# Performance work log

Hardware: AMD Instinct MI355X
Metric: run time of the kernel (lower is better)

Reference implementation:

```python
import jax, jax.numpy as jnp
import numpy as np

HEADS = 12  # hard-coded in the original module (rearrange h=12, temp shape (12,1))


def setup_inputs() -> dict:
    key = jax.random.key(0)
    k1, k2, k3 = jax.random.split(key, 3)
    B, C, H, W = 16, 768, 64, 64  # C = 3*dim with dim=256; per-head d = C/12 = 64
    x = jax.random.normal(k1, (B, C, H, W), dtype=jnp.float32)
    W_qkv = jax.random.normal(k2, (C, C), dtype=jnp.float32) * 0.02
    W_out = jax.random.normal(k3, (C, C), dtype=jnp.float32) * 0.02
    temp = jnp.ones((HEADS, 1), dtype=jnp.float32)
    return {"x": x, "W_qkv": W_qkv, "W_out": W_out, "temp": temp}


def reference(x, W_qkv, W_out, temp):
    B, C, H, W = x.shape
    N = H * W
    d = C // HEADS
    # to_3d: b c h w -> b (h w) c
    x3 = jnp.transpose(x, (0, 2, 3, 1)).reshape(B, N, C)
    # qkv projection (nn.Linear, no bias): x @ W^T
    w = (x3 @ W_qkv.T).reshape(B, N, HEADS, d).transpose(0, 2, 1, 3)  # [B, H, N, d]
    # F.normalize along the token axis (dim=-2), eps=1e-12
    norm = jnp.sqrt(jnp.sum(w * w, axis=2, keepdims=True))
    w_normed = w / jnp.maximum(norm, 1e-12)
    w_sq = w_normed ** 2
    # per-(head, token) stats, scaled by learned temp, softmax over HEADS axis (dim=1!)
    logits = jnp.sum(w_sq, axis=-1) * temp          # [B, H, N] (temp [12,1] broadcasts)
    Pi = jax.nn.softmax(logits, axis=1)             # softmax over heads
    Pi_n = Pi / (jnp.sum(Pi, axis=-1, keepdims=True) + 1e-8)
    # dots: [B,H,1,N] @ [B,H,N,d] -> [B,H,1,d]
    dots = jnp.einsum('bhn,bhnd->bhd', Pi_n, w ** 2)[:, :, None, :]
    attn = 1.0 / (1.0 + dots)                       # [B, H, 1, d]
    out = -(w * Pi[..., None]) * attn               # [B, H, N, d]
    # b h n d -> b n (h d)
    out = out.transpose(0, 2, 1, 3).reshape(B, N, C)
    out = out @ W_out.T
    # b (h w) c -> b c h w
    return out.reshape(B, H, W, C).transpose(0, 3, 1, 2)
```

## Files before the change

kernel.cpp:

```cpp
#include <hip/hip_runtime.h>
#include <stdint.h>

#define B_ 16
#define C_ 768
#define N_ 4096
#define HEADS_ 12

typedef __attribute__((ext_vector_type(4))) float f32x4;
typedef __attribute__((ext_vector_type(8))) short s16x8;

__device__ __forceinline__ ushort f2bf(float f){
  union { float f; uint32_t u; } v; v.f = f;
  uint32_t u = v.u;
  uint32_t r = (u + 0x7fffu + ((u >> 16) & 1u)) >> 16;
  return (ushort)r;
}
__device__ __forceinline__ float bf2f(ushort h){
  union { uint32_t u; float f; } v; v.u = ((uint32_t)h) << 16;
  return v.f;
}

__global__ __launch_bounds__(256) void k_convert(const float* __restrict__ src,
                                                 ushort* __restrict__ dst, int n){
  int i = (blockIdx.x * 256 + threadIdx.x) * 4;
  if (i < n){
    float4 v = *(const float4*)(src + i);
    ushort4 u;
    u.x = f2bf(v.x); u.y = f2bf(v.y); u.z = f2bf(v.z); u.w = f2bf(v.w);
    *(ushort4*)(dst + i) = u;
  }
}

__global__ __launch_bounds__(256) void k_transpose(const float* __restrict__ x,
                                                   ushort* __restrict__ xT){
  __shared__ ushort tile[64][72];
  int b = blockIdx.z;
  int n0 = blockIdx.x * 64;
  int k0 = blockIdx.y * 64;
  int t = threadIdx.x;
  const float* xb = x + (size_t)b * C_ * N_;
  #pragma unroll
  for (int p = 0; p < 4; ++p){
    int krow = (t >> 4) + p * 16;
    int nn = (t & 15) * 4;
    float4 v = *(const float4*)(xb + (size_t)(k0 + krow) * N_ + n0 + nn);
    tile[nn + 0][krow] = f2bf(v.x);
    tile[nn + 1][krow] = f2bf(v.y);
    tile[nn + 2][krow] = f2bf(v.z);
    tile[nn + 3][krow] = f2bf(v.w);
  }
  __syncthreads();
  ushort* dst = xT + (size_t)b * N_ * C_;
  #pragma unroll
  for (int p = 0; p < 4; ++p){
    int nrow = (t >> 4) + p * 16;
    int kk = (t & 15) * 4;
    ushort4 u = *(ushort4*)&tile[nrow][kk];
    *(ushort4*)(dst + (size_t)(n0 + nrow) * C_ + k0 + kk) = u;
  }
}

#define BM 128
#define BN 128
#define BK 64
#define LDK 72

__global__ __launch_bounds__(256, 2) void k_gemm1(const ushort* __restrict__ xT,
                                                  const ushort* __restrict__ wq,
                                                  ushort* __restrict__ w,
                                                  float* __restrict__ colnorm2){
  __shared__ ushort As[BM * LDK];
  __shared__ ushort Bs[BN * LDK];
  int b = blockIdx.z;
  int n0 = blockIdx.x * BM;
  int c0 = blockIdx.y * BN;
  int t = threadIdx.x;
  int lane = t & 63, wv = t >> 6;
  int wm = wv >> 1, wn = wv & 1;
  int col = lane & 15, quad = lane >> 4;
  const ushort* Ag = xT + (size_t)b * N_ * C_ + (size_t)n0 * C_;
  const ushort* Bg = wq + (size_t)c0 * C_;
  f32x4 acc[4][4] = {};
  for (int kt = 0; kt < C_; kt += BK){
    #pragma unroll
    for (int p = 0; p < 4; ++p){
      int q = t + 256 * p;
      int row = q >> 3, ch = q & 7;
      uint4 va = *(const uint4*)(Ag + (size_t)row * C_ + kt + ch * 8);
      *(uint4*)&As[row * LDK + ch * 8] = va;
      uint4 vb = *(const uint4*)(Bg + (size_t)row * C_ + kt + ch * 8);
      *(uint4*)&Bs[row * LDK + ch * 8] = vb;
    }
    __syncthreads();
    #pragma unroll
    for (int ks = 0; ks < 2; ++ks){
      s16x8 af[4], bf[4];
      #pragma unroll
      for (int mt = 0; mt < 4; ++mt)
        af[mt] = *(s16x8*)&As[(wm * 64 + mt * 16 + col) * LDK + ks * 32 + quad * 8];
      #pragma unroll
      for (int nt = 0; nt < 4; ++nt)
        bf[nt] = *(s16x8*)&Bs[(wn * 64 + nt * 16 + col) * LDK + ks * 32 + quad * 8];
      #pragma unroll
      for (int mt = 0; mt < 4; ++mt)
        #pragma unroll
        for (int nt = 0; nt < 4; ++nt)
          acc[mt][nt] = __builtin_amdgcn_mfma_f32_16x16x32_bf16(af[mt], bf[nt], acc[mt][nt], 0, 0, 0);
    }
    __syncthreads();
  }
  ushort* wb = w + (size_t)b * N_ * C_;
  #pragma unroll
  for (int nt = 0; nt < 4; ++nt){
    int cc = c0 + wn * 64 + nt * 16 + col;
    float ss = 0.f;
    #pragma unroll
    for (int mt = 0; mt < 4; ++mt){
      #pragma unroll
      for (int r = 0; r < 4; ++r){
        int nn = n0 + wm * 64 + mt * 16 + quad * 4 + r;
        float v = acc[mt][nt][r];
        wb[(size_t)nn * C_ + cc] = f2bf(v);
        ss += v * v;
      }
    }
    ss += __shfl_xor(ss, 16);
    ss += __shfl_xor(ss, 32);
    if (quad == 0) atomicAdd(colnorm2 + b * C_ + cc, ss);
  }
}

__global__ __launch_bounds__(256) void k_stats(const ushort* __restrict__ w,
                                               const float* __restrict__ colnorm2,
                                               const float* __restrict__ temp,
                                               float* __restrict__ Pi,
                                               float* __restrict__ S,
                                               float* __restrict__ T){
  int b = blockIdx.y;
  int chunk = blockIdx.x;
  int t = threadIdx.x;
  int lane = t & 63, wv = t >> 6;
  float invcn[HEADS_], tmp[HEADS_], S_loc[HEADS_], T_loc[HEADS_];
  #pragma unroll
  for (int j = 0; j < HEADS_; ++j){
    float cn = colnorm2[b * C_ + j * 64 + lane];
    invcn[j] = 1.0f / fmaxf(cn, 1e-24f);
    tmp[j] = temp[j];
    S_loc[j] = 0.f; T_loc[j] = 0.f;
  }
  const ushort* wb = w + (size_t)b * N_ * C_;
  for (int it = 0; it < 64; ++it){
    int n = chunk * 256 + wv * 64 + it;
    const ushort* row = wb + (size_t)n * C_;
    float v[HEADS_], r[HEADS_];
    #pragma unroll
    for (int j = 0; j < HEADS_; ++j){
      float f = bf2f(row[j * 64 + lane]);
      v[j] = f * f;
      r[j] = v[j] * invcn[j];
    }
    #pragma unroll
    for (int j = 0; j < HEADS_; ++j){
      #pragma unroll
      for (int off = 1; off < 64; off <<= 1)
        r[j] += __shfl_xor(r[j], off);
    }
    float m = -1e30f;
    #pragma unroll
    for (int j = 0; j < HEADS_; ++j){ r[j] *= tmp[j]; m = fmaxf(m, r[j]); }
    float se = 0.f, p[HEADS_];
    #pragma unroll
    for (int j = 0; j < HEADS_; ++j){ p[j] = __expf(r[j] - m); se += p[j]; }
    float inv = 1.0f / se;
    #pragma unroll
    for (int j = 0; j < HEADS_; ++j){
      p[j] *= inv;
      S_loc[j] += p[j];
      T_loc[j] += p[j] * v[j];
    }
    if (lane == 0){
      float4* dst = (float4*)(Pi + ((size_t)b * N_ + n) * HEADS_);
      dst[0] = make_float4(p[0], p[1], p[2], p[3]);
      dst[1] = make_float4(p[4], p[5], p[6], p[7]);
      dst[2] = make_float4(p[8], p[9], p[10], p[11]);
    }
  }
  #pragma unroll
  for (int j = 0; j < HEADS_; ++j){
    atomicAdd(T + b * C_ + j * 64 + lane, T_loc[j]);
    if (lane == j) atomicAdd(S + b * HEADS_ + j, S_loc[j]);
  }
}

__global__ __launch_bounds__(256) void k_attnfin(const float* __restrict__ S,
                                                 const float* __restrict__ T,
                                                 float* __restrict__ attn){
  int i = blockIdx.x * 256 + threadIdx.x;
  if (i < B_ * C_){
    int b = i / C_, c = i % C_;
    float dots = T[i] / (S[b * HEADS_ + c / 64] + 1e-8f);
    attn[i] = 1.0f / (1.0f + dots);
  }
}

__global__ __launch_bounds__(256, 2) void k_gemm2(const ushort* __restrict__ w,
                                                  const ushort* __restrict__ wout,
                                                  const float* __restrict__ Pi,
                                                  const float* __restrict__ attn,
                                                  float* __restrict__ out){
  __shared__ ushort As[BM * LDK];
  __shared__ ushort Bs[BN * LDK];
  int b = blockIdx.z;
  int c0 = blockIdx.x * BM;
  int n0 = blockIdx.y * BN;
  int t = threadIdx.x;
  int lane = t & 63, wv = t >> 6;
  int wm = wv >> 1, wn = wv & 1;
  int col = lane & 15, quad = lane >> 4;
  const ushort* Ag = wout + (size_t)c0 * C_;
  const ushort* Wg = w + (size_t)b * N_ * C_ + (size_t)n0 * C_;
  const float* attn_b = attn + b * C_;
  f32x4 acc[4][4] = {};
  for (int kt = 0; kt < HEADS_; ++kt){
    #pragma unroll
    for (int p = 0; p < 4; ++p){
      int q = t + 256 * p;
      int row = q >> 3, ch = q & 7;
      uint4 va = *(const uint4*)(Ag + (size_t)row * C_ + kt * 64 + ch * 8);
      *(uint4*)&As[row * LDK + ch * 8] = va;
      uint4 vb = *(const uint4*)(Wg + (size_t)row * C_ + kt * 64 + ch * 8);
      float pscale = -Pi[((size_t)b * N_ + n0 + row) * HEADS_ + kt];
      ushort* pv = (ushort*)&vb;
      ushort sc[8];
      #pragma unroll
      for (int i = 0; i < 8; ++i){
        float f = bf2f(pv[i]) * pscale * attn_b[kt * 64 + ch * 8 + i];
        sc[i] = f2bf(f);
      }
      *(uint4*)&Bs[row * LDK + ch * 8] = *(uint4*)sc;
    }
    __syncthreads();
    #pragma unroll
    for (int ks = 0; ks < 2; ++ks){
      s16x8 af[4], bf[4];
      #pragma unroll
      for (int mt = 0; mt < 4; ++mt)
        af[mt] = *(s16x8*)&As[(wm * 64 + mt * 16 + col) * LDK + ks * 32 + quad * 8];
      #pragma unroll
      for (int nt = 0; nt < 4; ++nt)
        bf[nt] = *(s16x8*)&Bs[(wn * 64 + nt * 16 + col) * LDK + ks * 32 + quad * 8];
      #pragma unroll
      for (int mt = 0; mt < 4; ++mt)
        #pragma unroll
        for (int nt = 0; nt < 4; ++nt)
          acc[mt][nt] = __builtin_amdgcn_mfma_f32_16x16x32_bf16(af[mt], bf[nt], acc[mt][nt], 0, 0, 0);
    }
    __syncthreads();
  }
  #pragma unroll
  for (int mt = 0; mt < 4; ++mt){
    #pragma unroll
    for (int nt = 0; nt < 4; ++nt){
      int nn = n0 + wn * 64 + nt * 16 + col;
      #pragma unroll
      for (int r = 0; r < 4; ++r){
        int cc = c0 + wm * 64 + mt * 16 + quad * 4 + r;
        out[((size_t)b * C_ + cc) * N_ + nn] = acc[mt][nt][r];
      }
    }
  }
}

extern "C" void kernel_launch(void* const* d_in, const int* in_sizes, int n_in,
                              void* d_out, int out_size, void* d_ws, size_t ws_size,
                              hipStream_t stream){
  const float* x    = (const float*)d_in[0];
  const float* Wqkv = (const float*)d_in[1];
  const float* Wout = (const float*)d_in[2];
  const float* temp = (const float*)d_in[3];
  float* out = (float*)d_out;
  char* ws = (char*)d_ws;

  const size_t sz_w  = (size_t)B_ * N_ * C_ * sizeof(ushort);
  const size_t sz_wt = (size_t)C_ * C_ * sizeof(ushort);

  ushort* w_buf = (ushort*)ws;
  ushort* wq_b  = (ushort*)(ws + sz_w);
  ushort* wo_b  = (ushort*)(ws + sz_w + sz_wt);
  float*  colnorm2 = (float*)(ws + sz_w + 2 * sz_wt);
  float*  S_ = colnorm2 + B_ * C_;
  float*  T_ = S_ + B_ * HEADS_;
  float*  Pi = T_ + B_ * C_;
  float*  attn = Pi + (size_t)B_ * N_ * HEADS_;
  ushort* xT = (ushort*)d_out;

  hipMemsetAsync(colnorm2, 0, (size_t)(2 * B_ * C_ + B_ * HEADS_) * sizeof(float), stream);

  k_convert<<<576, 256, 0, stream>>>(Wqkv, wq_b, C_ * C_);
  k_convert<<<576, 256, 0, stream>>>(Wout, wo_b, C_ * C_);
  k_transpose<<<dim3(N_ / 64, C_ / 64, B_), 256, 0, stream>>>(x, xT);
  k_gemm1<<<dim3(N_ / BM, C_ / BN, B_), 256, 0, stream>>>(xT, wq_b, w_buf, colnorm2);
  k_stats<<<dim3(16, B_), 256, 0, stream>>>(w_buf, colnorm2, temp, Pi, S_, T_);
  k_attnfin<<<48, 256, 0, stream>>>(S_, T_, attn);
  k_gemm2<<<dim3(C_ / BM, N_ / BN, B_), 256, 0, stream>>>(w_buf, wo_b, Pi, attn, out);
}
```

Before: 741.6 us.

## Fold attn into per-batch scaled W_out, write Pi-scaled w in place, use LDS-direct loads

The stats kernel now writes w*Pi back into the w buffer in bf16, so no separate Pi array is stored. The per-channel attn factor is folded into a per-batch scaled copy of W_out. This lets the second GEMM run a plain full-K bf16 GEMM with no per-element scaling while staging tiles. Both GEMMs now stage tiles with global_load_lds direct-to-LDS loads into unpadded shared arrays, which can add LDS bank conflicts. In exchange it needs a per-batch copy of W_out and an extra rounding step of w*Pi to bf16.

```diff
diff --git a/kernel.cpp b/kernel.cpp
--- a/kernel.cpp
+++ b/kernel.cpp
@@ -18,6 +18,12 @@
 __device__ __forceinline__ float bf2f(ushort h){
   union { uint32_t u; float f; } v; v.u = ((uint32_t)h) << 16;
   return v.f;
+}
+
+__device__ __forceinline__ void gload16(const ushort* g, ushort* l){
+  __builtin_amdgcn_global_load_lds(
+      (__attribute__((address_space(1))) void*)(g),
+      (__attribute__((address_space(3))) void*)(l), 16, 0, 0);
 }
 
 __global__ __launch_bounds__(256) void k_convert(const float* __restrict__ src,
@@ -63,14 +69,13 @@
 #define BM 128
 #define BN 128
 #define BK 64
-#define LDK 72
 
 __global__ __launch_bounds__(256, 2) void k_gemm1(const ushort* __restrict__ xT,
                                                   const ushort* __restrict__ wq,
                                                   ushort* __restrict__ w,
                                                   float* __restrict__ colnorm2){
-  __shared__ ushort As[BM * LDK];
-  __shared__ ushort Bs[BN * LDK];
+  __shared__ ushort As[BM * BK];
+  __shared__ ushort Bs[BN * BK];
   int b = blockIdx.z;
   int n0 = blockIdx.x * BM;
   int c0 = blockIdx.y * BN;
@@ -80,32 +85,32 @@
   int col = lane & 15, quad = lane >> 4;
   const ushort* Ag = xT + (size_t)b * N_ * C_ + (size_t)n0 * C_;
   const ushort* Bg = wq + (size_t)c0 * C_;
+  int srow = lane >> 3;
+  int sch  = (lane & 7) * 8;
   f32x4 acc[4][4] = {};
   for (int kt = 0; kt < C_; kt += BK){
     #pragma unroll
-    for (int p = 0; p < 4; ++p){
-      int q = t + 256 * p;
-      int row = q >> 3, ch = q & 7;
-      uint4 va = *(const uint4*)(Ag + (size_t)row * C_ + kt + ch * 8);
-      *(uint4*)&As[row * LDK + ch * 8] = va;
-      uint4 vb = *(const uint4*)(Bg + (size_t)row * C_ + kt + ch * 8);
-      *(uint4*)&Bs[row * LDK + ch * 8] = vb;
+    for (int c = 0; c < 4; ++c){
+      int rb8 = wv * 32 + c * 8;
+      int r = rb8 + srow;
+      gload16(Ag + (size_t)r * C_ + kt + sch, &As[rb8 * 64]);
+      gload16(Bg + (size_t)r * C_ + kt + sch, &Bs[rb8 * 64]);
     }
     __syncthreads();
     #pragma unroll
     for (int ks = 0; ks < 2; ++ks){
-      s16x8 af[4], bf[4];
+      s16x8 af[4], bfr[4];
       #pragma unroll
       for (int mt = 0; mt < 4; ++mt)
-        af[mt] = *(s16x8*)&As[(wm * 64 + mt * 16 + col) * LDK + ks * 32 + quad * 8];
+        af[mt] = *(const s16x8*)&As[(wm * 64 + mt * 16 + col) * 64 + ks * 32 + quad * 8];
       #pragma unroll
       for (int nt = 0; nt < 4; ++nt)
-        bf[nt] = *(s16x8*)&Bs[(wn * 64 + nt * 16 + col) * LDK + ks * 32 + quad * 8];
+        bfr[nt] = *(const s16x8*)&Bs[(wn * 64 + nt * 16 + col) * 64 + ks * 32 + quad * 8];
       #pragma unroll
       for (int mt = 0; mt < 4; ++mt)
         #pragma unroll
         for (int nt = 0; nt < 4; ++nt)
-          acc[mt][nt] = __builtin_amdgcn_mfma_f32_16x16x32_bf16(af[mt], bf[nt], acc[mt][nt], 0, 0, 0);
+          acc[mt][nt] = __builtin_amdgcn_mfma_f32_16x16x32_bf16(af[mt], bfr[nt], acc[mt][nt], 0, 0, 0);
     }
     __syncthreads();
   }
@@ -130,10 +135,9 @@
   }
 }
 
-__global__ __launch_bounds__(256) void k_stats(const ushort* __restrict__ w,
+__global__ __launch_bounds__(256) void k_stats(ushort* __restrict__ w,
                                                const float* __restrict__ colnorm2,
                                                const float* __restrict__ temp,
-                                               float* __restrict__ Pi,
                                                float* __restrict__ S,
                                                float* __restrict__ T){
   int b = blockIdx.y;
@@ -148,16 +152,16 @@
     tmp[j] = temp[j];
     S_loc[j] = 0.f; T_loc[j] = 0.f;
   }
-  const ushort* wb = w + (size_t)b * N_ * C_;
-  for (int it = 0; it < 64; ++it){
-    int n = chunk * 256 + wv * 64 + it;
-    const ushort* row = wb + (size_t)n * C_;
-    float v[HEADS_], r[HEADS_];
+  ushort* wb = w + (size_t)b * N_ * C_;
+  for (int it = 0; it < 32; ++it){
+    int n = chunk * 128 + wv * 32 + it;
+    ushort* row = wb + (size_t)n * C_;
+    float fj[HEADS_], r[HEADS_];
     #pragma unroll
     for (int j = 0; j < HEADS_; ++j){
       float f = bf2f(row[j * 64 + lane]);
-      v[j] = f * f;
-      r[j] = v[j] * invcn[j];
+      fj[j] = f;
+      r[j] = f * f * invcn[j];
     }
     #pragma unroll
     for (int j = 0; j < HEADS_; ++j){
@@ -176,13 +180,8 @@
     for (int j = 0; j < HEADS_; ++j){
       p[j] *= inv;
       S_loc[j] += p[j];
-      T_loc[j] += p[j] * v[j];
-    }
-    if (lane == 0){
-      float4* dst = (float4*)(Pi + ((size_t)b * N_ + n) * HEADS_);
-      dst[0] = make_float4(p[0], p[1], p[2], p[3]);
-      dst[1] = make_float4(p[4], p[5], p[6], p[7]);
-      dst[2] = make_float4(p[8], p[9], p[10], p[11]);
+      T_loc[j] += p[j] * fj[j] * fj[j];
+      row[j * 64 + lane] = f2bf(fj[j] * p[j]);
     }
   }
   #pragma unroll
@@ -192,68 +191,66 @@
   }
 }
 
-__global__ __launch_bounds__(256) void k_attnfin(const float* __restrict__ S,
-                                                 const float* __restrict__ T,
-                                                 float* __restrict__ attn){
-  int i = blockIdx.x * 256 + threadIdx.x;
-  if (i < B_ * C_){
-    int b = i / C_, c = i % C_;
-    float dots = T[i] / (S[b * HEADS_ + c / 64] + 1e-8f);
-    attn[i] = 1.0f / (1.0f + dots);
-  }
-}
-
-__global__ __launch_bounds__(256, 2) void k_gemm2(const ushort* __restrict__ w,
-                                                  const ushort* __restrict__ wout,
-                                                  const float* __restrict__ Pi,
-                                                  const float* __restrict__ attn,
-                                                  float* __restrict__ out){
-  __shared__ ushort As[BM * LDK];
-  __shared__ ushort Bs[BN * LDK];
-  int b = blockIdx.z;
+__global__ __launch_bounds__(256) void k_scale_wout(const float* __restrict__ Wout,
+                                                    const float* __restrict__ S,
+                                                    const float* __restrict__ T,
+                                                    ushort* __restrict__ woS,
+                                                    int b0){
+  int bz = blockIdx.y; int b = b0 + bz;
+  int i = (blockIdx.x * 256 + threadIdx.x) * 4;
+  int k = i % C_;
+  float s = S[b * HEADS_ + (k >> 6)] + 1e-8f;
+  float4 t4 = *(const float4*)(T + b * C_ + k);
+  float4 v = *(const float4*)(Wout + i);
+  ushort4 u;
+  u.x = f2bf(-v.x * s / (s + t4.x));
+  u.y = f2bf(-v.y * s / (s + t4.y));
+  u.z = f2bf(-v.z * s / (s + t4.z));
+  u.w = f2bf(-v.w * s / (s + t4.w));
+  *(ushort4*)(woS + (size_t)bz * C_ * C_ + i) = u;
+}
+
+__global__ __launch_bounds__(256, 2) void k_gemm2(const ushort* __restrict__ wp,
+                                                  const ushort* __restrict__ woS,
+                                                  float* __restrict__ out,
+                                                  int b0){
+  __shared__ ushort As[BM * BK];
+  __shared__ ushort Bs[BN * BK];
+  int bz = blockIdx.z; int b = b0 + bz;
   int c0 = blockIdx.x * BM;
   int n0 = blockIdx.y * BN;
   int t = threadIdx.x;
   int lane = t & 63, wv = t >> 6;
   int wm = wv >> 1, wn = wv & 1;
   int col = lane & 15, quad = lane >> 4;
-  const ushort* Ag = wout + (size_t)c0 * C_;
-  const ushort* Wg = w + (size_t)b * N_ * C_ + (size_t)n0 * C_;
-  const float* attn_b = attn + b * C_;
+  const ushort* Ag = woS + (size_t)bz * C_ * C_ + (size_t)c0 * C_;
+  const ushort* Bg = wp + (size_t)b * N_ * C_ + (size_t)n0 * C_;
+  int srow = lane >> 3;
+  int sch  = (lane & 7) * 8;
   f32x4 acc[4][4] = {};
-  for (int kt = 0; kt < HEADS_; ++kt){
-    #pragma unroll
-    for (int p = 0; p < 4; ++p){
-      int q = t + 256 * p;
-      int row = q >> 3, ch = q & 7;
-      uint4 va = *(const uint4*)(Ag + (size_t)row * C_ + kt * 64 + ch * 8);
-      *(uint4*)&As[row * LDK + ch * 8] = va;
-      uint4 vb = *(const uint4*)(Wg + (size_t)row * C_ + kt * 64 + ch * 8);
-      float pscale = -Pi[((size_t)b * N_ + n0 + row) * HEADS_ + kt];
-      ushort* pv = (ushort*)&vb;
-      ushort sc[8];
-      #pragma unroll
-      for (int i = 0; i < 8; ++i){
-        float f = bf2f(pv[i]) * pscale * attn_b[kt * 64 + ch * 8 + i];
-        sc[i] = f2bf(f);
-      }
-      *(uint4*)&Bs[row * LDK + ch * 8] = *(uint4*)sc;
+  for (int kt = 0; kt < C_; kt += BK){
+    #pragma unroll
+    for (int c = 0; c < 4; ++c){
+      int rb8 = wv * 32 + c * 8;
+      int r = rb8 + srow;
+      gload16(Ag + (size_t)r * C_ + kt + sch, &As[rb8 * 64]);
+      gload16(Bg + (size_t)r * C_ + kt + sch, &Bs[rb8 * 64]);
     }
     __syncthreads();
     #pragma unroll
     for (int ks = 0; ks < 2; ++ks){
-      s16x8 af[4], bf[4];
+      s16x8 af[4], bfr[4];
       #pragma unroll
       for (int mt = 0; mt < 4; ++mt)
-        af[mt] = *(s16x8*)&As[(wm * 64 + mt * 16 + col) * LDK + ks * 32 + quad * 8];
+        af[mt] = *(const s16x8*)&As[(wm * 64 + mt * 16 + col) * 64 + ks * 32 + quad * 8];
       #pragma unroll
       for (int nt = 0; nt < 4; ++nt)
-        bf[nt] = *(s16x8*)&Bs[(wn * 64 + nt * 16 + col) * LDK + ks * 32 + quad * 8];
+        bfr[nt] = *(const s16x8*)&Bs[(wn * 64 + nt * 16 + col) * 64 + ks * 32 + quad * 8];
       #pragma unroll
       for (int mt = 0; mt < 4; ++mt)
         #pragma unroll
         for (int nt = 0; nt < 4; ++nt)
-          acc[mt][nt] = __builtin_amdgcn_mfma_f32_16x16x32_bf16(af[mt], bf[nt], acc[mt][nt], 0, 0, 0);
+          acc[mt][nt] = __builtin_amdgcn_mfma_f32_16x16x32_bf16(af[mt], bfr[nt], acc[mt][nt], 0, 0, 0);
     }
     __syncthreads();
   }
@@ -281,26 +278,33 @@
   float* out = (float*)d_out;
   char* ws = (char*)d_ws;
 
-  const size_t sz_w  = (size_t)B_ * N_ * C_ * sizeof(ushort);
-  const size_t sz_wt = (size_t)C_ * C_ * sizeof(ushort);
-
-  ushort* w_buf = (ushort*)ws;
-  ushort* wq_b  = (ushort*)(ws + sz_w);
-  ushort* wo_b  = (ushort*)(ws + sz_w + sz_wt);
-  float*  colnorm2 = (float*)(ws + sz_w + 2 * sz_wt);
-  float*  S_ = colnorm2 + B_ * C_;
-  float*  T_ = S_ + B_ * HEADS_;
-  float*  Pi = T_ + B_ * C_;
-  float*  attn = Pi + (size_t)B_ * N_ * HEADS_;
-  ushort* xT = (ushort*)d_out;
-
-  hipMemsetAsync(colnorm2, 0, (size_t)(2 * B_ * C_ + B_ * HEADS_) * sizeof(float), stream);
-
+  const size_t sz_w     = (size_t)B_ * N_ * C_ * sizeof(ushort);
+  const size_t sz_wt    = (size_t)C_ * C_ * sizeof(ushort);
+  const size_t sz_stats = (size_t)(2 * B_ * C_ + B_ * HEADS_) * sizeof(float);
+
+  ushort* w_buf    = (ushort*)ws;
+  float*  colnorm2 = (float*)(ws + sz_w);
+  float*  S_       = colnorm2 + B_ * C_;
+  float*  T_       = S_ + B_ * HEADS_;
+  ushort* woS      = (ushort*)(ws + sz_w + sz_stats);
+
+  ushort* xT   = (ushort*)d_out;
+  ushort* wq_b = (ushort*)((char*)d_out + sz_w);
+
+  hipMemsetAsync(colnorm2, 0, sz_stats, stream);
   k_convert<<<576, 256, 0, stream>>>(Wqkv, wq_b, C_ * C_);
-  k_convert<<<576, 256, 0, stream>>>(Wout, wo_b, C_ * C_);
   k_transpose<<<dim3(N_ / 64, C_ / 64, B_), 256, 0, stream>>>(x, xT);
   k_gemm1<<<dim3(N_ / BM, C_ / BN, B_), 256, 0, stream>>>(xT, wq_b, w_buf, colnorm2);
-  k_stats<<<dim3(16, B_), 256, 0, stream>>>(w_buf, colnorm2, temp, Pi, S_, T_);
-  k_attnfin<<<48, 256, 0, stream>>>(S_, T_, attn);
-  k_gemm2<<<dim3(C_ / BM, N_ / BN, B_), 256, 0, stream>>>(w_buf, wo_b, Pi, attn, out);
-}
+  k_stats<<<dim3(32, B_), 256, 0, stream>>>(w_buf, colnorm2, temp, S_, T_);
+
+  const size_t need_full = sz_w + sz_stats + (size_t)B_ * sz_wt;
+  if (ws_size >= need_full){
+    k_scale_wout<<<dim3(C_ * C_ / 1024, B_), 256, 0, stream>>>(Wout, S_, T_, woS, 0);
+    k_gemm2<<<dim3(C_ / BM, N_ / BN, B_), 256, 0, stream>>>(w_buf, woS, out, 0);
+  } else {
+    for (int b0 = 0; b0 < B_; b0 += 4){
+      k_scale_wout<<<dim3(C_ * C_ / 1024, 4), 256, 0, stream>>>(Wout, S_, T_, woS, b0);
+      k_gemm2<<<dim3(C_ / BM, N_ / BN, 4), 256, 0, stream>>>(w_buf, woS, out, b0);
+    }
+  }
+}
```

Result: faster. 699.1 us (-5.7%).
